# Optimization experiments

Hardware: AMD Instinct MI355X
Metric: run time of the kernel (lower is better)

The kernel has to match this reference:

```python
import jax, jax.numpy as jnp
import numpy as np

D_MODEL = 1024
N_HEADS = 16
HEAD_DIM = 64
T = 4096
ROT = HEAD_DIM // 2          # 32 channels get rotary
PAIR = ROT // 2              # 16 cos/sin frequencies
EPS = 1e-6
SCALE = 0.12                 # constant attention scale (not 1/sqrt(d))
ROPE_BASE = 10000.0
VOCAB = 50257


def setup_inputs() -> dict:
    key = jax.random.key(0)
    k_x, k_qkv, k_o, k_tok = jax.random.split(key, 4)
    bound = 0.5 / np.sqrt(D_MODEL)
    x = jax.random.normal(k_x, (1, T, D_MODEL), dtype=jnp.float32)
    w_qkv = jax.random.uniform(k_qkv, (3 * D_MODEL, D_MODEL), jnp.float32, -bound, bound)
    # module uses zero_init for w_o; use small random so output is non-trivial
    w_o = jax.random.uniform(k_o, (D_MODEL, D_MODEL), jnp.float32, -bound, bound)
    q_norm_w = jnp.ones((HEAD_DIM,), jnp.float32)
    k_norm_w = jnp.ones((HEAD_DIM,), jnp.float32)
    tokens = jax.random.randint(k_tok, (1, T), 0, VOCAB, dtype=jnp.int64)
    pos = jnp.arange(T, dtype=jnp.int64)
    # RotaryCache: inv_freq over pair dims, cos/sin of t * inv_freq
    inv_freq = 1.0 / (ROPE_BASE ** (jnp.arange(PAIR, dtype=jnp.float32) / PAIR))
    freqs = jnp.arange(T, dtype=jnp.float32)[:, None] * inv_freq[None, :]  # [T, PAIR]
    return {
        "x": x, "tokens": tokens, "pos": pos,
        "w_qkv": w_qkv, "w_o": w_o,
        "q_norm_w": q_norm_w, "k_norm_w": k_norm_w,
        "cos": jnp.cos(freqs), "sin": jnp.sin(freqs),
        "window_tokens": 1024, "block_size": 128,
    }


def _rmsnorm(x, w):
    var = jnp.mean(x * x, axis=-1, keepdims=True)
    return x * jax.lax.rsqrt(var + EPS) * w


def reference(x, tokens, pos, w_qkv, w_o, q_norm_w, k_norm_w, cos, sin,
              window_tokens, block_size):
    B, Tq, C = x.shape
    H, Dh = N_HEADS, HEAD_DIM
    qkv = x @ w_qkv.T                                  # [B, T, 3C]
    q, k, v = jnp.split(qkv, 3, axis=-1)

    def to_bhtd(t):
        return t.reshape(B, Tq, H, Dh).transpose(0, 2, 1, 3)
    q, k, v = to_bhtd(q), to_bhtd(k), to_bhtd(v)

    q = _rmsnorm(q, q_norm_w)
    k = _rmsnorm(k, k_norm_w)

    # half-truncated RoPE: rotate first ROT channels pairwise (even/odd)
    c = cos[pos][None, None]                           # [1,1,T,PAIR]
    s = sin[pos][None, None]

    def rope_rotate(t):
        t1, t2 = t[..., :ROT], t[..., ROT:]
        even, odd = t1[..., 0::2], t1[..., 1::2]
        r_even = even * c - odd * s
        r_odd = even * s + odd * c
        t1r = jnp.stack([r_even, r_odd], axis=-1).reshape(t1.shape)
        return jnp.concatenate([t1r, t2], axis=-1)

    q = rope_rotate(q)
    k = rope_rotate(k)

    v = v * 0.5                                        # no value-embed branch

    scores = jnp.einsum('bhtd,bhsd->bhts', q, k) * SCALE
    idx = jnp.arange(Tq)
    diff = idx[:, None] - idx[None, :]
    allowed = (diff >= 0) & (diff < window_tokens)     # sliding causal window
    scores = jnp.where(allowed, scores, -jnp.inf)
    p = jax.nn.softmax(scores, axis=-1)
    out = jnp.einsum('bhts,bhsd->bhtd', p, v)
    out = out.transpose(0, 2, 1, 3).reshape(B, Tq, C)
    return out @ w_o.T
```

## Files before the change

### kernel.cpp

```cpp
#include <hip/hip_runtime.h>


typedef __bf16 bf16x8 __attribute__((ext_vector_type(8)));
typedef __bf16 bf16x2 __attribute__((ext_vector_type(2)));
typedef float f32x4 __attribute__((ext_vector_type(4)));
typedef unsigned short u16x8 __attribute__((ext_vector_type(8)));
typedef unsigned short u16x4 __attribute__((ext_vector_type(4)));

#define MFMA16(a, b, c) __builtin_amdgcn_mfma_f32_16x16x32_bf16((a), (b), (c), 0, 0, 0)

__device__ __forceinline__ unsigned short f2bf(float f) {
    unsigned int u = __float_as_uint(f);
    u += 0x7fffu + ((u >> 16) & 1u);
    return (unsigned short)(u >> 16);
}
__device__ __forceinline__ float bf2f(unsigned short h) {
    return __uint_as_float(((unsigned int)h) << 16);
}
__device__ __forceinline__ unsigned int pk2bf(float a, float b) {
#if __has_builtin(__builtin_amdgcn_cvt_pk_bf16_f32)
    bf16x2 v = __builtin_amdgcn_cvt_pk_bf16_f32(a, b);
    return __builtin_bit_cast(unsigned int, v);
#else
    return (unsigned int)f2bf(a) | ((unsigned int)f2bf(b) << 16);
#endif
}

__device__ __forceinline__ void gl_lds16(const void* g, void* l) {
    typedef __attribute__((address_space(1))) unsigned int GU;
    typedef __attribute__((address_space(3))) unsigned int LU;
    __builtin_amdgcn_global_load_lds((GU*)(unsigned long long)g,
                                     (LU*)(unsigned int)(unsigned long long)l,
                                     16, 0, 0);
}

__global__ void cvt3_kernel(const float* __restrict__ x,
                            const float* __restrict__ wqkv,
                            const float* __restrict__ wo,
                            unsigned short* __restrict__ xb,
                            unsigned short* __restrict__ wqkvb,
                            unsigned short* __restrict__ wob) {
    int i = blockIdx.x * 256 + threadIdx.x;
    const float* src;
    unsigned short* dst;
    int off;
    if (i < 1048576) { src = x; dst = xb; off = i; }
    else if (i < 1835008) { src = wqkv; dst = wqkvb; off = i - 1048576; }
    else { src = wo; dst = wob; off = i - 1835008; }
    float4 f = ((const float4*)src)[off];
    u16x4 o;
    o[0] = f2bf(f.x); o[1] = f2bf(f.y); o[2] = f2bf(f.z); o[3] = f2bf(f.w);
    ((u16x4*)dst)[off] = o;
}

__global__ __launch_bounds__(256) void gemm_qkv(
    const unsigned short* __restrict__ A,
    const unsigned short* __restrict__ Bt,
    const float* __restrict__ cosb, const float* __restrict__ sinb,
    const float* __restrict__ qw, const float* __restrict__ kw,
    unsigned short* __restrict__ Qb,
    unsigned short* __restrict__ Kb,
    unsigned short* __restrict__ Vt)
{
    __shared__ unsigned short As[128 * 32];
    __shared__ unsigned short Bs[128 * 32];
    __shared__ unsigned short tb[4][64 * 16];
    const int tid = threadIdx.x;
    const int wave = tid >> 6, lane = tid & 63;
    const int quad = lane >> 4, l16 = lane & 15;
    const int m0 = blockIdx.x * 128, n0 = blockIdx.y * 128;
    const int wm = (wave >> 1) * 64, wn = (wave & 1) * 64;
    (void)wn;

    f32x4 acc[4][4];
#pragma unroll
    for (int i = 0; i < 4; ++i)
#pragma unroll
        for (int j = 0; j < 4; ++j) acc[i][j] = (f32x4){0.f, 0.f, 0.f, 0.f};

    for (int k0 = 0; k0 < 1024; k0 += 32) {
#pragma unroll
        for (int i = 0; i < 2; ++i) {
            const int c = wave * 2 + i;
            const int e = (c * 64 + lane) * 8;
            const int r = e >> 5, col = e & 31;
            gl_lds16(A + (size_t)(m0 + r) * 1024 + (k0 + col), &As[c * 512]);
            gl_lds16(Bt + (size_t)(n0 + r) * 1024 + (k0 + col), &Bs[c * 512]);
        }
        __syncthreads();
        bf16x8 af[4], bfr[4];
#pragma unroll
        for (int mt = 0; mt < 4; ++mt)
            af[mt] = *(const bf16x8*)&As[(wm + mt * 16 + l16) * 32 + quad * 8];
#pragma unroll
        for (int nt = 0; nt < 4; ++nt)
            bfr[nt] = *(const bf16x8*)&Bs[((wave & 1) * 64 + nt * 16 + l16) * 32 + quad * 8];
#pragma unroll
        for (int mt = 0; mt < 4; ++mt)
#pragma unroll
            for (int nt = 0; nt < 4; ++nt)
                acc[mt][nt] = MFMA16(af[mt], bfr[nt], acc[mt][nt]);
        __syncthreads();
    }

    const int region = blockIdx.y >> 3;
    const int h = ((blockIdx.y & 7) << 1) + (wave & 1);

    if (region < 2) {
        const float* wgt = region ? kw : qw;
        unsigned short* dst = region ? Kb : Qb;
        float w[4];
#pragma unroll
        for (int nt = 0; nt < 4; ++nt) w[nt] = wgt[nt * 16 + l16];
#pragma unroll
        for (int mt = 0; mt < 4; ++mt)
#pragma unroll
            for (int r = 0; r < 4; ++r) {
                const int row = m0 + wm + mt * 16 + quad * 4 + r;
                float ss = 0.f;
#pragma unroll
                for (int nt = 0; nt < 4; ++nt)
                    ss += acc[mt][nt][r] * acc[mt][nt][r];
                ss += __shfl_xor(ss, 1); ss += __shfl_xor(ss, 2);
                ss += __shfl_xor(ss, 4); ss += __shfl_xor(ss, 8);
                const float rn = rsqrtf(ss * (1.f / 64.f) + 1e-6f);
                float val[4];
#pragma unroll
                for (int nt = 0; nt < 4; ++nt)
                    val[nt] = acc[mt][nt][r] * rn * w[nt];
#pragma unroll
                for (int nt = 0; nt < 2; ++nt) {
                    const float prt = __shfl_xor(val[nt], 1);
                    const int p = nt * 8 + (l16 >> 1);
                    const float c = cosb[row * 16 + p];
                    const float s = sinb[row * 16 + p];
                    val[nt] = (l16 & 1) ? (prt * s + val[nt] * c)
                                        : (val[nt] * c - prt * s);
                }
                const size_t ob = ((size_t)h * 4096 + row) * 64;
#pragma unroll
                for (int nt = 0; nt < 4; ++nt)
                    dst[ob + nt * 16 + l16] = f2bf(val[nt]);
            }
    } else {
        unsigned short* tbw = tb[wave];
#pragma unroll
        for (int mt = 0; mt < 4; ++mt) {
#pragma unroll
            for (int nt = 0; nt < 4; ++nt)
#pragma unroll
                for (int r = 0; r < 4; ++r)
                    tbw[(nt * 16 + l16) * 16 + quad * 4 + r] =
                        f2bf(acc[mt][nt][r] * 0.5f);
            u16x8 v0 = *(const u16x8*)&tbw[lane * 16];
            u16x8 v1 = *(const u16x8*)&tbw[lane * 16 + 8];
            const size_t vo = ((size_t)h * 64 + lane) * 4096 + m0 + wm + mt * 16;
            *(u16x8*)&Vt[vo] = v0;
            *(u16x8*)&Vt[vo + 8] = v1;
        }
    }
}

#define PSTR 72

template <int MODE>
__device__ __forceinline__ void attn_step(
    int s0, int tq, int wave, int quad, int l16, int krow, int kcol,
    const unsigned short* __restrict__ Kh, const unsigned short* __restrict__ Vh,
    unsigned short* Ks0, unsigned short* Ks1,
    unsigned short* Vs0, unsigned short* Vs1, unsigned short* Pw,
    const bf16x8 qf0, const bf16x8 qf1, f32x4 (&o)[4], float& lsum)
{
    __syncthreads();
    const unsigned short* kb = Kh + (size_t)(s0 + krow) * 64 + kcol;
    const unsigned short* vb = Vh + (size_t)krow * 4096 + s0 + kcol;
    gl_lds16(kb,      &Ks0[wave * 512]);
    gl_lds16(kb + 32, &Ks1[wave * 512]);
    gl_lds16(vb,      &Vs0[wave * 512]);
    gl_lds16(vb + 32, &Vs1[wave * 512]);
    __syncthreads();

    const float c = 0.17312340490667046f;
#pragma unroll
    for (int i = 0; i < 4; ++i) {
        const bf16x8 kf0 = *(const bf16x8*)&Ks0[(i * 16 + l16) * 32 + quad * 8];
        const bf16x8 kf1 = *(const bf16x8*)&Ks1[(i * 16 + l16) * 32 + quad * 8];
        f32x4 z = (f32x4){0.f, 0.f, 0.f, 0.f};
        z = MFMA16(kf0, qf0, z);
        z = MFMA16(kf1, qf1, z);
        float p[4];
#pragma unroll
        for (int r = 0; r < 4; ++r) {
            float e = exp2f(z[r] * c);
            if (MODE == 1) {
                const int s = s0 + i * 16 + quad * 4 + r;
                e = ((tq - s) < 1024) ? e : 0.f;
            }
            if (MODE == 2) {
                const int s = s0 + i * 16 + quad * 4 + r;
                e = (s <= tq) ? e : 0.f;
            }
            p[r] = e;
            lsum += e;
        }
        uint2 pk;
        pk.x = pk2bf(p[0], p[1]);
        pk.y = pk2bf(p[2], p[3]);
        *(uint2*)&Pw[l16 * PSTR + i * 16 + quad * 4] = pk;
    }
    const bf16x8 pf0 = *(const bf16x8*)&Pw[l16 * PSTR + quad * 8];
    const bf16x8 pf1 = *(const bf16x8*)&Pw[l16 * PSTR + 32 + quad * 8];
#pragma unroll
    for (int dt = 0; dt < 4; ++dt) {
        const bf16x8 vf0 = *(const bf16x8*)&Vs0[(dt * 16 + l16) * 32 + quad * 8];
        const bf16x8 vf1 = *(const bf16x8*)&Vs1[(dt * 16 + l16) * 32 + quad * 8];
        o[dt] = MFMA16(pf0, vf0, o[dt]);
        o[dt] = MFMA16(pf1, vf1, o[dt]);
    }
}

__global__ __launch_bounds__(256) void attn_kernel(
    const unsigned short* __restrict__ Qb,
    const unsigned short* __restrict__ Kb,
    const unsigned short* __restrict__ Vt,
    unsigned short* __restrict__ att)
{
    __shared__ unsigned short Ks0[64 * 32];
    __shared__ unsigned short Ks1[64 * 32];
    __shared__ unsigned short Vs0[64 * 32];
    __shared__ unsigned short Vs1[64 * 32];
    __shared__ unsigned short P[4][16 * PSTR];

    const int bid = blockIdx.x;
    const int h = ((bid & 7) << 1) | ((bid >> 3) & 1);
    const int t0 = (bid >> 4) * 64;

    const int tid = threadIdx.x;
    const int wave = tid >> 6, lane = tid & 63;
    const int quad = lane >> 4, l16 = lane & 15;
    const int qt0 = t0 + wave * 16;
    const int tq = qt0 + l16;
    const int krow = tid >> 2, kcol = (tid & 3) * 8;

    const unsigned short* Qh = Qb + (size_t)h * 4096 * 64;
    const unsigned short* Kh = Kb + (size_t)h * 4096 * 64;
    const unsigned short* Vh = Vt + (size_t)h * 64 * 4096;

    const bf16x8 qf0 = *(const bf16x8*)&Qh[(qt0 + l16) * 64 + quad * 8];
    const bf16x8 qf1 = *(const bf16x8*)&Qh[(qt0 + l16) * 64 + 32 + quad * 8];

    f32x4 o[4];
#pragma unroll
    for (int dt = 0; dt < 4; ++dt) o[dt] = (f32x4){0.f, 0.f, 0.f, 0.f};
    float lsum = 0.f;
    unsigned short* Pw = P[wave];

    int s0 = (t0 >= 1024) ? (t0 - 1024) : 0;
    if (t0 >= 1024) {
        attn_step<1>(s0, tq, wave, quad, l16, krow, kcol, Kh, Vh,
                     Ks0, Ks1, Vs0, Vs1, Pw, qf0, qf1, o, lsum);
        s0 += 64;
    }
    for (; s0 < t0; s0 += 64)
        attn_step<0>(s0, tq, wave, quad, l16, krow, kcol, Kh, Vh,
                     Ks0, Ks1, Vs0, Vs1, Pw, qf0, qf1, o, lsum);
    attn_step<2>(t0, tq, wave, quad, l16, krow, kcol, Kh, Vh,
                 Ks0, Ks1, Vs0, Vs1, Pw, qf0, qf1, o, lsum);

    lsum += __shfl_xor(lsum, 16);
    lsum += __shfl_xor(lsum, 32);
    float lr[4];
#pragma unroll
    for (int r = 0; r < 4; ++r) lr[r] = 1.f / __shfl(lsum, quad * 4 + r);
#pragma unroll
    for (int dt = 0; dt < 4; ++dt)
#pragma unroll
        for (int r = 0; r < 4; ++r)
            att[(size_t)(qt0 + quad * 4 + r) * 1024 + h * 64 + dt * 16 + l16] =
                f2bf(o[dt][r] * lr[r]);
}

template <int BM, bool F32OUT>
__global__ __launch_bounds__(256) void gemm_bt(
    const unsigned short* __restrict__ A,
    const unsigned short* __restrict__ Bt,
    void* __restrict__ Cp, int N, int K) {
    __shared__ unsigned short As[BM * 32];
    __shared__ unsigned short Bs[128 * 32];
    constexpr int MT = BM / 32;
    const int tid = threadIdx.x;
    const int wave = tid >> 6, lane = tid & 63;
    const int quad = lane >> 4, l16 = lane & 15;
    const int m0 = blockIdx.x * BM, n0 = blockIdx.y * 128;
    const int wm = (wave >> 1) * (BM / 2), wn = (wave & 1) * 64;

    f32x4 acc[MT][4];
#pragma unroll
    for (int i = 0; i < MT; ++i)
#pragma unroll
        for (int j = 0; j < 4; ++j) acc[i][j] = (f32x4){0.f, 0.f, 0.f, 0.f};

    for (int k0 = 0; k0 < K; k0 += 32) {
#pragma unroll
        for (int i = 0; i < BM / 64; ++i) {
            const int c = wave * (BM / 64) + i;
            const int e = (c * 64 + lane) * 8;
            const int r = e >> 5, col = e & 31;
            gl_lds16(A + (size_t)(m0 + r) * K + (k0 + col), &As[c * 512]);
        }
#pragma unroll
        for (int i = 0; i < 2; ++i) {
            const int c = wave * 2 + i;
            const int e = (c * 64 + lane) * 8;
            const int r = e >> 5, col = e & 31;
            gl_lds16(Bt + (size_t)(n0 + r) * K + (k0 + col), &Bs[c * 512]);
        }
        __syncthreads();
        bf16x8 af[MT], bfr[4];
#pragma unroll
        for (int mt = 0; mt < MT; ++mt)
            af[mt] = *(const bf16x8*)&As[(wm + mt * 16 + l16) * 32 + quad * 8];
#pragma unroll
        for (int nt = 0; nt < 4; ++nt)
            bfr[nt] = *(const bf16x8*)&Bs[(wn + nt * 16 + l16) * 32 + quad * 8];
#pragma unroll
        for (int mt = 0; mt < MT; ++mt)
#pragma unroll
            for (int nt = 0; nt < 4; ++nt)
                acc[mt][nt] = MFMA16(af[mt], bfr[nt], acc[mt][nt]);
        __syncthreads();
    }
#pragma unroll
    for (int mt = 0; mt < MT; ++mt)
#pragma unroll
        for (int nt = 0; nt < 4; ++nt)
#pragma unroll
            for (int r = 0; r < 4; ++r) {
                const int row = m0 + wm + mt * 16 + quad * 4 + r;
                const int col = n0 + wn + nt * 16 + l16;
                const float v = acc[mt][nt][r];
                if (F32OUT)
                    ((float*)Cp)[(size_t)row * N + col] = v;
                else
                    ((unsigned short*)Cp)[(size_t)row * N + col] = f2bf(v);
            }
}

extern "C" void kernel_launch(void* const* d_in, const int* in_sizes, int n_in,
                              void* d_out, int out_size, void* d_ws, size_t ws_size,
                              hipStream_t stream) {
    const float* x    = (const float*)d_in[0];
    const float* wqkv = (const float*)d_in[3];
    const float* wo   = (const float*)d_in[4];
    const float* qw   = (const float*)d_in[5];
    const float* kw   = (const float*)d_in[6];
    const float* cosb = (const float*)d_in[7];
    const float* sinb = (const float*)d_in[8];

    char* ws = (char*)d_ws;
    if (ws_size < (size_t)48 * 1024 * 1024) return;
    unsigned short* xb    = (unsigned short*)(ws + ((size_t)0 << 20));
    unsigned short* wqkvb = (unsigned short*)(ws + ((size_t)8 << 20));
    unsigned short* wob   = (unsigned short*)(ws + ((size_t)14 << 20));
    unsigned short* Qb    = (unsigned short*)(ws + ((size_t)16 << 20));
    unsigned short* Kb    = (unsigned short*)(ws + ((size_t)24 << 20));
    unsigned short* Vt    = (unsigned short*)(ws + ((size_t)32 << 20));
    unsigned short* attb  = (unsigned short*)(ws + ((size_t)40 << 20));

    cvt3_kernel<<<8192, 256, 0, stream>>>(x, wqkv, wo, xb, wqkvb, wob);

    gemm_qkv<<<dim3(32, 24), 256, 0, stream>>>(xb, wqkvb, cosb, sinb, qw, kw,
                                               Qb, Kb, Vt);

    attn_kernel<<<1024, 256, 0, stream>>>(Qb, Kb, Vt, attb);

    gemm_bt<64, true><<<dim3(64, 8), 256, 0, stream>>>(attb, wob, (float*)d_out, 1024, 1024);
}
```

Measured before the change: 209.0 us.

## Shrink QKV GEMM tile, stage Q/K stores via LDS, fold scale into Q, reverse attention order

The QKV GEMM tile drops from 128x128 to 64x128 and the grid doubles, giving more blocks across the CUs, with an occupancy hint added to launch bounds. Q/K results are now staged through LDS so each row is written with 16-byte vector stores instead of scattered 2-byte stores. The softmax scale times log2(e) is folded into the Q norm weight, so the attention inner loop uses a raw hardware exp2 with no multiply. Attention blocks are issued in reverse time order so the heavier late-query tiles start first. The smaller tile lowers operand reuse per block, and folding the scale into Q before the bf16 rounding slightly changes numerics.

```diff
diff --git a/kernel.cpp b/kernel.cpp
--- a/kernel.cpp
+++ b/kernel.cpp
@@ -23,6 +23,13 @@
     return __builtin_bit_cast(unsigned int, v);
 #else
     return (unsigned int)f2bf(a) | ((unsigned int)f2bf(b) << 16);
+#endif
+}
+__device__ __forceinline__ float fexp2(float x) {
+#if __has_builtin(__builtin_amdgcn_exp2f)
+    return __builtin_amdgcn_exp2f(x);
+#else
+    return exp2f(x);
 #endif
 }
 
@@ -53,7 +60,8 @@
     ((u16x4*)dst)[off] = o;
 }
 
-__global__ __launch_bounds__(256) void gemm_qkv(
+#define TBS 72
+__global__ __launch_bounds__(256, 6) void gemm_qkv(
     const unsigned short* __restrict__ A,
     const unsigned short* __restrict__ Bt,
     const float* __restrict__ cosb, const float* __restrict__ sinb,
@@ -62,41 +70,44 @@
     unsigned short* __restrict__ Kb,
     unsigned short* __restrict__ Vt)
 {
-    __shared__ unsigned short As[128 * 32];
+    __shared__ unsigned short As[64 * 32];
     __shared__ unsigned short Bs[128 * 32];
-    __shared__ unsigned short tb[4][64 * 16];
+    __shared__ unsigned short tb[4][16 * TBS];
     const int tid = threadIdx.x;
     const int wave = tid >> 6, lane = tid & 63;
     const int quad = lane >> 4, l16 = lane & 15;
-    const int m0 = blockIdx.x * 128, n0 = blockIdx.y * 128;
-    const int wm = (wave >> 1) * 64, wn = (wave & 1) * 64;
-    (void)wn;
-
-    f32x4 acc[4][4];
-#pragma unroll
-    for (int i = 0; i < 4; ++i)
+    const int m0 = blockIdx.x * 64, n0 = blockIdx.y * 128;
+    const int wm = (wave >> 1) * 32, wn = (wave & 1) * 64;
+
+    f32x4 acc[2][4];
+#pragma unroll
+    for (int i = 0; i < 2; ++i)
 #pragma unroll
         for (int j = 0; j < 4; ++j) acc[i][j] = (f32x4){0.f, 0.f, 0.f, 0.f};
 
     for (int k0 = 0; k0 < 1024; k0 += 32) {
+        {
+            const int e = (wave * 64 + lane) * 8;
+            const int r = e >> 5, col = e & 31;
+            gl_lds16(A + (size_t)(m0 + r) * 1024 + (k0 + col), &As[wave * 512]);
+        }
 #pragma unroll
         for (int i = 0; i < 2; ++i) {
             const int c = wave * 2 + i;
             const int e = (c * 64 + lane) * 8;
             const int r = e >> 5, col = e & 31;
-            gl_lds16(A + (size_t)(m0 + r) * 1024 + (k0 + col), &As[c * 512]);
             gl_lds16(Bt + (size_t)(n0 + r) * 1024 + (k0 + col), &Bs[c * 512]);
         }
         __syncthreads();
-        bf16x8 af[4], bfr[4];
-#pragma unroll
-        for (int mt = 0; mt < 4; ++mt)
+        bf16x8 af[2], bfr[4];
+#pragma unroll
+        for (int mt = 0; mt < 2; ++mt)
             af[mt] = *(const bf16x8*)&As[(wm + mt * 16 + l16) * 32 + quad * 8];
 #pragma unroll
         for (int nt = 0; nt < 4; ++nt)
-            bfr[nt] = *(const bf16x8*)&Bs[((wave & 1) * 64 + nt * 16 + l16) * 32 + quad * 8];
-#pragma unroll
-        for (int mt = 0; mt < 4; ++mt)
+            bfr[nt] = *(const bf16x8*)&Bs[(wn + nt * 16 + l16) * 32 + quad * 8];
+#pragma unroll
+        for (int mt = 0; mt < 2; ++mt)
 #pragma unroll
             for (int nt = 0; nt < 4; ++nt)
                 acc[mt][nt] = MFMA16(af[mt], bfr[nt], acc[mt][nt]);
@@ -105,15 +116,17 @@
 
     const int region = blockIdx.y >> 3;
     const int h = ((blockIdx.y & 7) << 1) + (wave & 1);
+    unsigned short* tbw = tb[wave];
 
     if (region < 2) {
         const float* wgt = region ? kw : qw;
         unsigned short* dst = region ? Kb : Qb;
+        const float post = region ? 1.f : 0.17312340490667046f;
         float w[4];
 #pragma unroll
-        for (int nt = 0; nt < 4; ++nt) w[nt] = wgt[nt * 16 + l16];
-#pragma unroll
-        for (int mt = 0; mt < 4; ++mt)
+        for (int nt = 0; nt < 4; ++nt) w[nt] = wgt[nt * 16 + l16] * post;
+#pragma unroll
+        for (int mt = 0; mt < 2; ++mt) {
 #pragma unroll
             for (int r = 0; r < 4; ++r) {
                 const int row = m0 + wm + mt * 16 + quad * 4 + r;
@@ -137,15 +150,20 @@
                     val[nt] = (l16 & 1) ? (prt * s + val[nt] * c)
                                         : (val[nt] * c - prt * s);
                 }
-                const size_t ob = ((size_t)h * 4096 + row) * 64;
 #pragma unroll
                 for (int nt = 0; nt < 4; ++nt)
-                    dst[ob + nt * 16 + l16] = f2bf(val[nt]);
+                    tbw[(quad * 4 + r) * TBS + nt * 16 + l16] = f2bf(val[nt]);
             }
+            const int t = lane >> 2, dcol = (lane & 3) * 16;
+            u16x8 v0 = *(const u16x8*)&tbw[t * TBS + dcol];
+            u16x8 v1 = *(const u16x8*)&tbw[t * TBS + dcol + 8];
+            const size_t ob = ((size_t)h * 4096 + (m0 + wm + mt * 16 + t)) * 64 + dcol;
+            *(u16x8*)&dst[ob] = v0;
+            *(u16x8*)&dst[ob + 8] = v1;
+        }
     } else {
-        unsigned short* tbw = tb[wave];
-#pragma unroll
-        for (int mt = 0; mt < 4; ++mt) {
+#pragma unroll
+        for (int mt = 0; mt < 2; ++mt) {
 #pragma unroll
             for (int nt = 0; nt < 4; ++nt)
 #pragma unroll
@@ -180,7 +198,6 @@
     gl_lds16(vb + 32, &Vs1[wave * 512]);
     __syncthreads();
 
-    const float c = 0.17312340490667046f;
 #pragma unroll
     for (int i = 0; i < 4; ++i) {
         const bf16x8 kf0 = *(const bf16x8*)&Ks0[(i * 16 + l16) * 32 + quad * 8];
@@ -191,7 +208,7 @@
         float p[4];
 #pragma unroll
         for (int r = 0; r < 4; ++r) {
-            float e = exp2f(z[r] * c);
+            float e = fexp2(z[r]);
             if (MODE == 1) {
                 const int s = s0 + i * 16 + quad * 4 + r;
                 e = ((tq - s) < 1024) ? e : 0.f;
@@ -233,7 +250,7 @@
 
     const int bid = blockIdx.x;
     const int h = ((bid & 7) << 1) | ((bid >> 3) & 1);
-    const int t0 = (bid >> 4) * 64;
+    const int t0 = (63 - (bid >> 4)) * 64;
 
     const int tid = threadIdx.x;
     const int wave = tid >> 6, lane = tid & 63;
@@ -369,7 +386,7 @@
 
     cvt3_kernel<<<8192, 256, 0, stream>>>(x, wqkv, wo, xb, wqkvb, wob);
 
-    gemm_qkv<<<dim3(32, 24), 256, 0, stream>>>(xb, wqkvb, cosb, sinb, qw, kw,
+    gemm_qkv<<<dim3(64, 24), 256, 0, stream>>>(xb, wqkvb, cosb, sinb, qw, kw,
                                                Qb, Kb, Vt);
 
     attn_kernel<<<1024, 256, 0, stream>>>(Qb, Kb, Vt, attb);
```

After: 197.4 us. -5.5%, faster.
